# Kernel tuning notes

Measured on AMD Instinct MI355X. Metric: run time of the kernel, lower is better.

## Reference

```python
import jax, jax.numpy as jnp
import numpy as np

# Irreps config: input/output = 32x0e + 16x1o (dim 80), H=4 heads -> head = 8x0e + 4x1o (dim 20)
M0, M1 = 32, 16      # input muls for 0e / 1o
m0, m1 = 8, 4        # per-head muls
H = 4
HEAD_DIM = m0 + 3 * m1   # 20
WNUM = H * (M0 * m0 + M1 * m0 + M0 * m1 + M1 * m1)  # 2304 per-edge TP weights
NB, HID = 16, 64
SQRT3 = np.float32(np.sqrt(3.0))
EPS = 1e-8


def radial_mlp(x, W1, b1, W2, b2):
    return jax.nn.silu(x @ W1 + b1) @ W2 + b2


def tp_edge(ss, vv, sh0, sh1, w):
    """FullyConnectedTensorProduct (32x0e+16x1o) x (1x0e+1x1o) -> H*(8x0e+4x1o) with per-edge weights w [E, WNUM].
    Paths: 0e*0e->0e, 1o*1o->0e (CG dot/sqrt3), 0e*1o->1o, 1o*0e->1o; path norm 1/sqrt(fan_in)."""
    E = ss.shape[0]
    per = M0 * m0 + M1 * m0 + M0 * m1 + M1 * m1  # 576
    w = w.reshape(E, H, per)
    o = 0
    Wss = w[..., o:o + M0 * m0].reshape(E, H, M0, m0); o += M0 * m0
    Wvv = w[..., o:o + M1 * m0].reshape(E, H, M1, m0); o += M1 * m0
    Wsv = w[..., o:o + M0 * m1].reshape(E, H, M0, m1); o += M0 * m1
    Wvs = w[..., o:o + M1 * m1].reshape(E, H, M1, m1)
    fan = np.float32(np.sqrt(M0 + M1))  # fan_in = 48 for both output irreps
    vv_dot = jnp.einsum('eui,ei->eu', vv, sh1) / SQRT3
    out0 = (jnp.einsum('eu,ehuw->ehw', ss * sh0[:, None], Wss)
            + jnp.einsum('eu,ehuw->ehw', vv_dot, Wvv)) / fan          # [E,H,m0]
    out1 = (jnp.einsum('eu,ehuw->ehw', ss, Wsv)[..., None] * sh1[:, None, None, :]
            + jnp.einsum('eui,ehuw->ehwi', vv * sh0[:, None, None], Wvs)) / fan  # [E,H,m1,3]
    return out0, out1


def setup_inputs() -> dict:
    key = jax.random.key(0)
    ks = jax.random.split(key, 24)
    N, E = 2000, 32000
    g = lambda k, s, sc=1.0: jax.random.normal(k, s, jnp.float32) * sc
    inp = {}
    inp['node_features'] = g(ks[0], (N, M0 + 3 * M1))
    inp['edge_index'] = jax.random.randint(ks[1], (2, E), 0, N)
    inp['edge_sh'] = g(ks[2], (E, 4))
    inp['edge_radial_emb'] = jax.random.uniform(ks[3], (E, NB), jnp.float32)
    # query e3nn Linear (per-head blocks)
    inp['Wq0'] = g(ks[4], (H, M0, m0))
    inp['Wq1'] = g(ks[5], (H, M1, m1))
    # radial MLPs for key / value TP weights
    inp['Wk1'] = g(ks[6], (NB, HID), 1 / np.sqrt(NB)); inp['bk1'] = jnp.zeros((HID,), jnp.float32)
    inp['Wk2'] = g(ks[7], (HID, WNUM), 1 / np.sqrt(HID)); inp['bk2'] = jnp.zeros((WNUM,), jnp.float32)
    inp['Wv1'] = g(ks[8], (NB, HID), 1 / np.sqrt(NB)); inp['bv1'] = jnp.zeros((HID,), jnp.float32)
    inp['Wv2'] = g(ks[9], (HID, WNUM), 1 / np.sqrt(HID)); inp['bv2'] = jnp.zeros((WNUM,), jnp.float32)
    # single-head dot-product TP -> 0e (shared weights)
    inp['Wd0'] = g(ks[10], (m0, m0))
    inp['Wd1'] = g(ks[11], (m1, m1))
    # output projection Linear (all heads mixed per irrep)
    inp['Wo0'] = g(ks[12], (H * m0, M0))
    inp['Wo1'] = g(ks[13], (H * m1, M1))
    # FFN: out irreps -> (2*M0)x0e + M1x1o -> out irreps
    inp['Wf1_0'] = g(ks[14], (M0, 2 * M0))
    inp['Wf1_1'] = g(ks[15], (M1, M1))
    inp['Wf2_0'] = g(ks[16], (2 * M0, M0))
    inp['Wf2_1'] = g(ks[17], (M1, M1))
    return inp


def reference(node_features, edge_index, edge_sh, edge_radial_emb,
              Wq0, Wq1, Wk1, bk1, Wk2, bk2, Wv1, bv1, Wv2, bv2,
              Wd0, Wd1, Wo0, Wo1, Wf1_0, Wf1_1, Wf2_0, Wf2_1):
    N = node_features.shape[0]
    s = node_features[:, :M0]                       # [N, M0] scalars
    v = node_features[:, M0:].reshape(N, M1, 3)     # [N, M1, 3] vectors
    src, dst = edge_index[0], edge_index[1]

    # query Linear (e3nn: per-irrep channel mix, norm 1/sqrt(fan_in))
    q0 = jnp.einsum('nu,huw->nhw', s, Wq0) / np.sqrt(M0)
    q1 = jnp.einsum('nui,huw->nhwi', v, Wq1) / np.sqrt(M1)

    sh0, sh1 = edge_sh[:, 0], edge_sh[:, 1:4]
    ss, vv = s[src], v[src]                         # gather per edge

    wk = radial_mlp(edge_radial_emb, Wk1, bk1, Wk2, bk2)
    wv = radial_mlp(edge_radial_emb, Wv1, bv1, Wv2, bv2)
    k0, k1 = tp_edge(ss, vv, sh0, sh1, wk)
    v0, v1 = tp_edge(ss, vv, sh0, sh1, wv)

    # per-head equivariant dot product -> 0e logits
    qd0, qd1 = q0[dst], q1[dst]
    fan_d = np.float32(np.sqrt(m0 * m0 + m1 * m1))
    logits = (jnp.einsum('ehu,uv,ehv->eh', qd0, Wd0, k0)
              + jnp.einsum('ehui,uv,ehvi->eh', qd1, Wd1, k1) / SQRT3) / fan_d
    logits = logits / np.sqrt(HEAD_DIM)             # self.scale
    logits = jnp.clip(logits, -10.0, 10.0)

    # scatter softmax over edges sharing a destination node
    seg_max = jax.ops.segment_max(logits, dst, num_segments=N)
    seg_max = jnp.maximum(seg_max, -10.0)           # handle empty segments
    ex = jnp.exp(logits - seg_max[dst])
    denom = jax.ops.segment_sum(ex, dst, num_segments=N)
    alpha = ex / (denom[dst] + 1e-12)               # [E, H]

    agg0 = jax.ops.segment_sum(alpha[..., None] * v0, dst, num_segments=N)        # [N,H,m0]
    agg1 = jax.ops.segment_sum(alpha[..., None, None] * v1, dst, num_segments=N)  # [N,H,m1,3]

    # output projection Linear over concatenated heads
    o0 = agg0.reshape(N, H * m0) @ Wo0 / np.sqrt(H * m0)
    o1 = jnp.einsum('nui,uw->nwi', agg1.reshape(N, H * m1, 3), Wo1) / np.sqrt(H * m1)

    # residual (input irreps == output irreps -> identity skip)
    x0 = s + o0
    x1 = v + o1

    # FFN with SafeNormActivation
    f0 = x0 @ Wf1_0 / np.sqrt(M0)                               # [N, 2*M0]
    f1 = jnp.einsum('nui,uw->nwi', x1, Wf1_1) / np.sqrt(M1)     # [N, M1, 3]
    a0 = jax.nn.silu(f0)
    norms = jnp.linalg.norm(f1, axis=-1, keepdims=True)
    safe = jnp.maximum(norms, EPS)
    a1 = jnp.where(norms < EPS, 0.0, (f1 / safe) * jax.nn.silu(norms))
    g0 = a0 @ Wf2_0 / np.sqrt(2 * M0)
    g1 = jnp.einsum('nui,uw->nwi', a1, Wf2_1) / np.sqrt(M1)

    out0 = x0 + g0
    out1 = x1 + g1
    return jnp.concatenate([out0, out1.reshape(N, M1 * 3)], axis=-1)
```

## Files before the change

### kernel.cpp

```cpp
#include <hip/hip_runtime.h>

typedef unsigned int uint;
typedef unsigned short ushort;
typedef __attribute__((ext_vector_type(8))) short bf16x8;
typedef __attribute__((ext_vector_type(4))) float f32x4;

#define N_NODES 2000
#define N_EDGES 32000
#define WNUM 2304

constexpr size_t OFF_AGG0 = 0;
constexpr size_t OFF_AGG1 = 64000;
constexpr size_t OFF_DEN  = 160000;
constexpr size_t OFF_FLAG = 168000;
constexpr size_t OFF_W2T  = 168004;

__device__ __forceinline__ float b2f(ushort u){ union{uint i; float f;}x; x.i=((uint)u)<<16; return x.f; }
__device__ __forceinline__ ushort f2b(float f){
  union{float f; uint u;}x; x.f=f;
  uint r = (x.u + 0x7FFFu + ((x.u>>16)&1u)) >> 16;
  return (ushort)r;
}
__device__ __forceinline__ float siluf(float x){ return x / (1.f + __expf(-x)); }

template<bool F32>
__device__ __forceinline__ float ldf(const void* p, int i){
  if (F32) return ((const float*)p)[i];
  return b2f(((const ushort*)p)[i]);
}
__device__ __forceinline__ float ldfr(const void* p, int i, bool f32){
  return f32 ? ((const float*)p)[i] : b2f(((const ushort*)p)[i]);
}

__global__ void probe_kernel(const ushort* __restrict__ nf, int* __restrict__ flag){
  __shared__ int cnt;
  if (threadIdx.x == 0) cnt = 0;
  __syncthreads();
  uint u = nf[threadIdx.x * 2];
  uint ex = (u >> 7) & 0xFFu;
  if (ex >= 0xA0u) atomicAdd(&cnt, 1);
  __syncthreads();
  if (threadIdx.x == 0) *flag = (cnt >= 20) ? 1 : 0;
}

__global__ __launch_bounds__(256) void w2t_kernel(const void* __restrict__ Wk2,
                                                  const void* __restrict__ Wv2,
                                                  ushort* __restrict__ W2T,
                                                  const int* __restrict__ flag){
  const bool F32 = (*flag) != 0;
  int id = blockIdx.x*256 + threadIdx.x;
  int mat = id / 147456;
  int rem = id - mat*147456;
  int c = rem & 63, j = rem >> 6;
  const void* W = mat ? Wv2 : Wk2;
  float v = F32 ? ((const float*)W)[c*WNUM + j] : b2f(((const ushort*)W)[c*WNUM + j]);
  W2T[id] = f2b(v);
}

struct Smem {
  ushort hidA[2][32][64];
  float fssT[32][32];
  float fvvT[16][32];
  float sslT[32][32];
  float vshT[16][3][32];
  float qd0T[4][8][32];
  float qd1T[4][4][3][32];
  float sh1T[3][32];
  float dstF[32][80];
  int   dstL[32];
};

template<bool F32>
__device__ void edge_body(
    const void* __restrict__ nf,  const int* __restrict__ eidx,
    const void* __restrict__ esh, const void* __restrict__ emb,
    const void* __restrict__ Wk1, const void* __restrict__ bk1, const void* __restrict__ bk2,
    const void* __restrict__ Wv1, const void* __restrict__ bv1, const void* __restrict__ bv2,
    const void* __restrict__ Wq0, const void* __restrict__ Wq1,
    const void* __restrict__ Wd0, const void* __restrict__ Wd1,
    const ushort* __restrict__ W2T,
    float* __restrict__ agg0, float* __restrict__ agg1, float* __restrict__ denom,
    Smem& sm){
  const int t  = threadIdx.x;
  const int hw = t >> 5;
  const int r  = t & 31;
  const int geb = blockIdx.x*32;

  #pragma unroll 1
  for (int e=0; e<4; ++e){
    const int le = hw*4+e, ge = geb+le;
    const int src = eidx[ge], d = eidx[N_EDGES+ge];
    const float sh0 = ldf<F32>(esh, ge*4+0);
    const float s1a = ldf<F32>(esh, ge*4+1), s1b = ldf<F32>(esh, ge*4+2), s1c = ldf<F32>(esh, ge*4+3);
    if (r == 0) sm.dstL[le] = d;
    if (r < 3) sm.sh1T[r][le] = (r==0)? s1a : (r==1)? s1b : s1c;
    float sv = ldf<F32>(nf, src*80 + r);
    sm.sslT[r][le] = sv;
    sm.fssT[r][le] = sv * sh0;
    sm.dstF[le][r] = ldf<F32>(nf, d*80 + r);
    if (r < 16){
      float v0 = ldf<F32>(nf, src*80+32+r*3+0);
      float v1 = ldf<F32>(nf, src*80+32+r*3+1);
      float v2 = ldf<F32>(nf, src*80+32+r*3+2);
      sm.vshT[r][0][le] = v0*sh0; sm.vshT[r][1][le] = v1*sh0; sm.vshT[r][2][le] = v2*sh0;
      sm.fvvT[r][le] = (v0*s1a + v1*s1b + v2*s1c) * 0.5773502691896258f;
      sm.dstF[le][32+r*3+0] = ldf<F32>(nf, d*80+32+r*3+0);
      sm.dstF[le][32+r*3+1] = ldf<F32>(nf, d*80+32+r*3+1);
      sm.dstF[le][32+r*3+2] = ldf<F32>(nf, d*80+32+r*3+2);
    }
  }

  #pragma unroll 1
  for (int e=0; e<4; ++e){
    const int le = hw*4+e;
    const int h8 = r & 24, w8 = r & 7;
    float a = 0.f;
    #pragma unroll
    for (int u=0; u<32; ++u) a += sm.dstF[le][u] * ldf<F32>(Wq0, (r>>3)*256 + u*8 + w8);
    const float q0 = a * 0.17677669529663687f;
    float qd0 = 0.f;
    #pragma unroll
    for (int u=0; u<8; ++u) qd0 += __shfl(q0, h8+u, 32) * ldf<F32>(Wd0, u*8 + w8);
    sm.qd0T[r>>3][w8][le] = qd0;

    const int rr = r & 15, h4 = rr>>2, w4 = rr&3;
    float q1i[3];
    #pragma unroll
    for (int i=0; i<3; ++i){
      float b = 0.f;
      #pragma unroll
      for (int u=0; u<16; ++u) b += sm.dstF[le][32+u*3+i] * ldf<F32>(Wq1, h4*64 + u*4 + w4);
      q1i[i] = b * 0.25f;
    }
    #pragma unroll
    for (int i=0; i<3; ++i){
      float b = 0.f;
      #pragma unroll
      for (int u=0; u<4; ++u) b += __shfl(q1i[i], h4*4+u, 32) * ldf<F32>(Wd1, u*4 + w4);
      if (r < 16) sm.qd1T[h4][w4][i][le] = b;
    }
  }

  #pragma unroll 1
  for (int e=0; e<4; ++e){
    const int le = hw*4+e, ge = geb+le;
    float em[16];
    #pragma unroll
    for (int b=0; b<16; ++b) em[b] = ldf<F32>(emb, ge*16 + b);
    #pragma unroll
    for (int cc=0; cc<2; ++cc){
      const int c = r + cc*32;
      float ak = ldf<F32>(bk1, c), av = ldf<F32>(bv1, c);
      #pragma unroll
      for (int b=0; b<16; ++b){
        ak += em[b] * ldf<F32>(Wk1, b*64 + c);
        av += em[b] * ldf<F32>(Wv1, b*64 + c);
      }
      sm.hidA[0][le][c] = f2b(siluf(ak));
      sm.hidA[1][le][c] = f2b(siluf(av));
    }
  }
  __syncthreads();

  const int h = t >> 6;
  const int lane = t & 63, q = lane >> 4, n = lane & 15;
  const ushort* w2tk = W2T;
  const ushort* w2tv = W2T + 147456;

  bf16x8 af[2][2][2];
  #pragma unroll
  for (int kv=0; kv<2; ++kv)
    #pragma unroll
    for (int Mt=0; Mt<2; ++Mt)
      #pragma unroll
      for (int kh=0; kh<2; ++kh)
        af[kv][Mt][kh] = *(const bf16x8*)&sm.hidA[kv][Mt*16+n][kh*32 + q*8];

  float aK0[2][4], aV0[2][4], aPK[2][4], aPV[2][4], aWK[3][2][4], aWV[3][2][4];
  #pragma unroll
  for (int Mt=0; Mt<2; ++Mt)
    #pragma unroll
    for (int z=0; z<4; ++z){
      aK0[Mt][z]=0.f; aV0[Mt][z]=0.f; aPK[Mt][z]=0.f; aPV[Mt][z]=0.f;
      aWK[0][Mt][z]=0.f; aWK[1][Mt][z]=0.f; aWK[2][Mt][z]=0.f;
      aWV[0][Mt][z]=0.f; aWV[1][Mt][z]=0.f; aWV[2][Mt][z]=0.f;
    }

  #pragma unroll 2
  for (int tl=0; tl<16; ++tl){
    const size_t tb = ((size_t)((h*36+tl)*16 + n))*64 + q*8;
    bf16x8 bk0 = *(const bf16x8*)(w2tk + tb), bk1f = *(const bf16x8*)(w2tk + tb + 32);
    bf16x8 bv0 = *(const bf16x8*)(w2tv + tb), bv1f = *(const bf16x8*)(w2tv + tb + 32);
    const int j = h*576 + tl*16 + n;
    const float bbk = ldf<F32>(bk2, j), bbv = ldf<F32>(bv2, j);
    const int u = tl*2 + (n>>3);
    #pragma unroll
    for (int Mt=0; Mt<2; ++Mt){
      f32x4 fv = *(const f32x4*)&sm.fssT[u][Mt*16+q*4];
      f32x4 ck = {bbk,bbk,bbk,bbk};
      ck = __builtin_amdgcn_mfma_f32_16x16x32_bf16(af[0][Mt][0], bk0, ck, 0,0,0);
      ck = __builtin_amdgcn_mfma_f32_16x16x32_bf16(af[0][Mt][1], bk1f, ck, 0,0,0);
      f32x4 cv = {bbv,bbv,bbv,bbv};
      cv = __builtin_amdgcn_mfma_f32_16x16x32_bf16(af[1][Mt][0], bv0, cv, 0,0,0);
      cv = __builtin_amdgcn_mfma_f32_16x16x32_bf16(af[1][Mt][1], bv1f, cv, 0,0,0);
      #pragma unroll
      for (int z=0; z<4; ++z){ aK0[Mt][z] += ck[z]*fv[z]; aV0[Mt][z] += cv[z]*fv[z]; }
    }
  }
  #pragma unroll 2
  for (int tl=16; tl<24; ++tl){
    const size_t tb = ((size_t)((h*36+tl)*16 + n))*64 + q*8;
    bf16x8 bk0 = *(const bf16x8*)(w2tk + tb), bk1f = *(const bf16x8*)(w2tk + tb + 32);
    bf16x8 bv0 = *(const bf16x8*)(w2tv + tb), bv1f = *(const bf16x8*)(w2tv + tb + 32);
    const int j = h*576 + tl*16 + n;
    const float bbk = ldf<F32>(bk2, j), bbv = ldf<F32>(bv2, j);
    const int u = (tl-16)*2 + (n>>3);
    #pragma unroll
    for (int Mt=0; Mt<2; ++Mt){
      f32x4 fv = *(const f32x4*)&sm.fvvT[u][Mt*16+q*4];
      f32x4 ck = {bbk,bbk,bbk,bbk};
      ck = __builtin_amdgcn_mfma_f32_16x16x32_bf16(af[0][Mt][0], bk0, ck, 0,0,0);
      ck = __builtin_amdgcn_mfma_f32_16x16x32_bf16(af[0][Mt][1], bk1f, ck, 0,0,0);
      f32x4 cv = {bbv,bbv,bbv,bbv};
      cv = __builtin_amdgcn_mfma_f32_16x16x32_bf16(af[1][Mt][0], bv0, cv, 0,0,0);
      cv = __builtin_amdgcn_mfma_f32_16x16x32_bf16(af[1][Mt][1], bv1f, cv, 0,0,0);
      #pragma unroll
      for (int z=0; z<4; ++z){ aK0[Mt][z] += ck[z]*fv[z]; aV0[Mt][z] += cv[z]*fv[z]; }
    }
  }
  #pragma unroll 2
  for (int tl=24; tl<32; ++tl){
    const size_t tb = ((size_t)((h*36+tl)*16 + n))*64 + q*8;
    bf16x8 bk0 = *(const bf16x8*)(w2tk + tb), bk1f = *(const bf16x8*)(w2tk + tb + 32);
    bf16x8 bv0 = *(const bf16x8*)(w2tv + tb), bv1f = *(const bf16x8*)(w2tv + tb + 32);
    const int j = h*576 + tl*16 + n;
    const float bbk = ldf<F32>(bk2, j), bbv = ldf<F32>(bv2, j);
    const int u = (tl-24)*4 + (n>>2);
    #pragma unroll
    for (int Mt=0; Mt<2; ++Mt){
      f32x4 fv = *(const f32x4*)&sm.sslT[u][Mt*16+q*4];
      f32x4 ck = {bbk,bbk,bbk,bbk};
      ck = __builtin_amdgcn_mfma_f32_16x16x32_bf16(af[0][Mt][0], bk0, ck, 0,0,0);
      ck = __builtin_amdgcn_mfma_f32_16x16x32_bf16(af[0][Mt][1], bk1f, ck, 0,0,0);
      f32x4 cv = {bbv,bbv,bbv,bbv};
      cv = __builtin_amdgcn_mfma_f32_16x16x32_bf16(af[1][Mt][0], bv0, cv, 0,0,0);
      cv = __builtin_amdgcn_mfma_f32_16x16x32_bf16(af[1][Mt][1], bv1f, cv, 0,0,0);
      #pragma unroll
      for (int z=0; z<4; ++z){ aPK[Mt][z] += ck[z]*fv[z]; aPV[Mt][z] += cv[z]*fv[z]; }
    }
  }
  #pragma unroll 1
  for (int tl=32; tl<36; ++tl){
    const size_t tb = ((size_t)((h*36+tl)*16 + n))*64 + q*8;
    bf16x8 bk0 = *(const bf16x8*)(w2tk + tb), bk1f = *(const bf16x8*)(w2tk + tb + 32);
    bf16x8 bv0 = *(const bf16x8*)(w2tv + tb), bv1f = *(const bf16x8*)(w2tv + tb + 32);
    const int j = h*576 + tl*16 + n;
    const float bbk = ldf<F32>(bk2, j), bbv = ldf<F32>(bv2, j);
    const int u = (tl-32)*4 + (n>>2);
    #pragma unroll
    for (int Mt=0; Mt<2; ++Mt){
      f32x4 ck = {bbk,bbk,bbk,bbk};
      ck = __builtin_amdgcn_mfma_f32_16x16x32_bf16(af[0][Mt][0], bk0, ck, 0,0,0);
      ck = __builtin_amdgcn_mfma_f32_16x16x32_bf16(af[0][Mt][1], bk1f, ck, 0,0,0);
      f32x4 cv = {bbv,bbv,bbv,bbv};
      cv = __builtin_amdgcn_mfma_f32_16x16x32_bf16(af[1][Mt][0], bv0, cv, 0,0,0);
      cv = __builtin_amdgcn_mfma_f32_16x16x32_bf16(af[1][Mt][1], bv1f, cv, 0,0,0);
      #pragma unroll
      for (int i=0; i<3; ++i){
        f32x4 fv = *(const f32x4*)&sm.vshT[u][i][Mt*16+q*4];
        #pragma unroll
        for (int z=0; z<4; ++z){ aWK[i][Mt][z] += ck[z]*fv[z]; aWV[i][Mt][z] += cv[z]*fv[z]; }
      }
    }
  }

  #pragma unroll
  for (int Mt=0; Mt<2; ++Mt)
    #pragma unroll
    for (int z=0; z<4; ++z){
      aK0[Mt][z] += __shfl_xor(aK0[Mt][z], 8, 64);
      aV0[Mt][z] += __shfl_xor(aV0[Mt][z], 8, 64);
      aPK[Mt][z] += __shfl_xor(aPK[Mt][z], 4, 64);
      aPK[Mt][z] += __shfl_xor(aPK[Mt][z], 8, 64);
      aPV[Mt][z] += __shfl_xor(aPV[Mt][z], 4, 64);
      aPV[Mt][z] += __shfl_xor(aPV[Mt][z], 8, 64);
      #pragma unroll
      for (int i=0; i<3; ++i){
        aWK[i][Mt][z] += __shfl_xor(aWK[i][Mt][z], 4, 64);
        aWK[i][Mt][z] += __shfl_xor(aWK[i][Mt][z], 8, 64);
        aWV[i][Mt][z] += __shfl_xor(aWV[i][Mt][z], 4, 64);
        aWV[i][Mt][z] += __shfl_xor(aWV[i][Mt][z], 8, 64);
      }
    }

  const float invfan = 0.14433756729740643f;
  f32x4 s1v[3][2];
  #pragma unroll
  for (int i=0; i<3; ++i)
    #pragma unroll
    for (int Mt=0; Mt<2; ++Mt)
      s1v[i][Mt] = *(const f32x4*)&sm.sh1T[i][Mt*16+q*4];

  float lgp[2][4];
  #pragma unroll
  for (int Mt=0; Mt<2; ++Mt){
    f32x4 qd0v = *(const f32x4*)&sm.qd0T[h][n&7][Mt*16+q*4];
    #pragma unroll
    for (int z=0; z<4; ++z){
      float acc = (n < 8) ? qd0v[z]*aK0[Mt][z] : 0.f;
      if (n < 4){
        float s = 0.f;
        #pragma unroll
        for (int i=0; i<3; ++i){
          f32x4 qd1v = *(const f32x4*)&sm.qd1T[h][n&3][i][Mt*16+q*4];
          float k1 = aPK[Mt][z]*s1v[i][Mt][z] + aWK[i][Mt][z];
          s += qd1v[z]*k1;
        }
        acc += s * 0.5773502691896258f;
      }
      lgp[Mt][z] = acc;
    }
  }
  #pragma unroll
  for (int Mt=0; Mt<2; ++Mt)
    #pragma unroll
    for (int z=0; z<4; ++z){
      lgp[Mt][z] += __shfl_xor(lgp[Mt][z], 1, 64);
      lgp[Mt][z] += __shfl_xor(lgp[Mt][z], 2, 64);
      lgp[Mt][z] += __shfl_xor(lgp[Mt][z], 4, 64);
      lgp[Mt][z] += __shfl_xor(lgp[Mt][z], 8, 64);
    }

  float exv[2][4]; int dn[2][4];
  #pragma unroll
  for (int Mt=0; Mt<2; ++Mt)
    #pragma unroll
    for (int z=0; z<4; ++z){
      float lg = lgp[Mt][z] * invfan * 0.025f;
      lg = fminf(10.f, fmaxf(-10.f, lg));
      exv[Mt][z] = __expf(lg - 10.0f);
      dn[Mt][z] = sm.dstL[Mt*16 + q*4 + z];
    }

  if (n == 0){
    #pragma unroll
    for (int Mt=0; Mt<2; ++Mt)
      #pragma unroll
      for (int z=0; z<4; ++z)
        atomicAdd(denom + dn[Mt][z]*4 + h, exv[Mt][z]);
  }
  if (n < 8){
    #pragma unroll
    for (int Mt=0; Mt<2; ++Mt)
      #pragma unroll
      for (int z=0; z<4; ++z)
        atomicAdd(agg0 + dn[Mt][z]*32 + h*8 + n, exv[Mt][z]*aV0[Mt][z]*invfan);
  }
  if (n < 4){
    #pragma unroll
    for (int i=0; i<3; ++i)
      #pragma unroll
      for (int Mt=0; Mt<2; ++Mt)
        #pragma unroll
        for (int z=0; z<4; ++z){
          float v1 = (aPV[Mt][z]*s1v[i][Mt][z] + aWV[i][Mt][z]) * invfan;
          atomicAdd(agg1 + dn[Mt][z]*48 + h*12 + n*3 + i, exv[Mt][z]*v1);
        }
  }
}

__global__ __launch_bounds__(256) void edge_kernel(
    const void* nf, const int* eidx, const void* esh, const void* emb,
    const void* Wk1, const void* bk1, const void* bk2,
    const void* Wv1, const void* bv1, const void* bv2,
    const void* Wq0, const void* Wq1, const void* Wd0, const void* Wd1,
    const ushort* W2T, float* agg0, float* agg1, float* denom, const int* flag){
  __shared__ Smem sm;
  if (*flag)
    edge_body<true >(nf,eidx,esh,emb,Wk1,bk1,bk2,Wv1,bv1,bv2,Wq0,Wq1,Wd0,Wd1,W2T,agg0,agg1,denom,sm);
  else
    edge_body<false>(nf,eidx,esh,emb,Wk1,bk1,bk2,Wv1,bv1,bv2,Wq0,Wq1,Wd0,Wd1,W2T,agg0,agg1,denom,sm);
}

__global__ __launch_bounds__(64) void node_out_kernel(
    const void* __restrict__ nf, const float* __restrict__ agg0r, const float* __restrict__ agg1r,
    const float* __restrict__ denom,
    const void* __restrict__ Wo0, const void* __restrict__ Wo1,
    const void* __restrict__ Wf10, const void* __restrict__ Wf11,
    const void* __restrict__ Wf20, const void* __restrict__ Wf21,
    void* __restrict__ out, const int* __restrict__ flag){
  __shared__ float ag0[32], ag1[48], adiv[4];
  __shared__ float x0s[32], x1s[48], a0s[64], f1s[48], coefs[16];
  const bool F32 = (*flag) != 0;
  const int n = blockIdx.x, t = threadIdx.x;
  if (t < 4) adiv[t] = 1.f / (denom[n*4+t] + 1e-12f);
  __syncthreads();
  if (t < 32) ag0[t] = agg0r[n*32+t] * adiv[t>>3];
  if (t < 48) ag1[t] = agg1r[n*48+t] * adiv[t/12];
  __syncthreads();
  if (t < 32){
    float o = 0.f;
    #pragma unroll
    for (int k=0; k<32; ++k) o += ag0[k]*ldfr(Wo0, k*32+t, F32);
    x0s[t] = ldfr(nf, n*80+t, F32) + o*0.17677669529663687f;
  }
  if (t < 48){
    int w = t/3, i = t - w*3;
    float o = 0.f;
    #pragma unroll
    for (int u=0; u<16; ++u) o += ag1[u*3+i]*ldfr(Wo1, u*16+w, F32);
    x1s[t] = ldfr(nf, n*80+32+t, F32) + o*0.25f;
  }
  __syncthreads();
  {
    float f0 = 0.f;
    #pragma unroll
    for (int u=0; u<32; ++u) f0 += x0s[u]*ldfr(Wf10, u*64+t, F32);
    a0s[t] = siluf(f0*0.17677669529663687f);
  }
  if (t < 48){
    int w = t/3, i = t - w*3;
    float f1 = 0.f;
    #pragma unroll
    for (int u=0; u<16; ++u) f1 += x1s[u*3+i]*ldfr(Wf11, u*16+w, F32);
    f1s[t] = f1*0.25f;
  }
  __syncthreads();
  if (t < 16){
    float a = f1s[t*3], b = f1s[t*3+1], c = f1s[t*3+2];
    float nrm = sqrtf(a*a+b*b+c*c);
    float safe = fmaxf(nrm, 1e-8f);
    coefs[t] = (nrm < 1e-8f) ? 0.f : siluf(nrm)/safe;
  }
  __syncthreads();
  if (t < 32){
    float g = 0.f;
    #pragma unroll
    for (int u=0; u<64; ++u) g += a0s[u]*ldfr(Wf20, u*32+t, F32);
    float val = x0s[t] + g*0.125f;
    if (F32) ((float*)out)[n*80+t] = val; else ((ushort*)out)[n*80+t] = f2b(val);
  }
  if (t < 48){
    int w = t/3, i = t - w*3;
    float g = 0.f;
    #pragma unroll
    for (int u=0; u<16; ++u) g += coefs[u]*f1s[u*3+i]*ldfr(Wf21, u*16+w, F32);
    float val = x1s[t] + g*0.25f;
    if (F32) ((float*)out)[n*80+32+t] = val; else ((ushort*)out)[n*80+32+t] = f2b(val);
  }
}

extern "C" void kernel_launch(void* const* d_in, const int* in_sizes, int n_in,
                              void* d_out, int out_size, void* d_ws, size_t ws_size,
                              hipStream_t stream){
  const void* nf   = d_in[0];
  const int*  eidx = (const int*)d_in[1];
  const void* esh  = d_in[2];
  const void* emb  = d_in[3];
  const void* Wq0  = d_in[4];
  const void* Wq1  = d_in[5];
  const void* Wk1  = d_in[6];
  const void* bk1  = d_in[7];
  const void* Wk2  = d_in[8];
  const void* bk2  = d_in[9];
  const void* Wv1  = d_in[10];
  const void* bv1  = d_in[11];
  const void* Wv2  = d_in[12];
  const void* bv2  = d_in[13];
  const void* Wd0  = d_in[14];
  const void* Wd1  = d_in[15];
  const void* Wo0  = d_in[16];
  const void* Wo1  = d_in[17];
  const void* Wf10 = d_in[18];
  const void* Wf11 = d_in[19];
  const void* Wf20 = d_in[20];
  const void* Wf21 = d_in[21];
  float* ws = (float*)d_ws;

  float* agg0  = ws + OFF_AGG0;
  float* agg1  = ws + OFF_AGG1;
  float* denom = ws + OFF_DEN;
  int*   flag  = (int*)(ws + OFF_FLAG);
  ushort* W2T  = (ushort*)(ws + OFF_W2T);

  hipMemsetAsync(agg0, 0, (64000+96000+8000)*sizeof(float), stream);
  probe_kernel<<<1, 256, 0, stream>>>((const ushort*)nf, flag);
  w2t_kernel<<<1152, 256, 0, stream>>>(Wk2, Wv2, W2T, flag);
  edge_kernel<<<N_EDGES/32, 256, 0, stream>>>(nf, eidx, esh, emb,
                                              Wk1, bk1, bk2, Wv1, bv1, bv2,
                                              Wq0, Wq1, Wd0, Wd1, W2T,
                                              agg0, agg1, denom, flag);
  node_out_kernel<<<N_NODES, 64, 0, stream>>>(nf, agg0, agg1, denom,
                                              Wo0, Wo1, Wf10, Wf11, Wf20, Wf21, d_out, flag);
}
```

Baseline: 244.2 us.

## Precompute per-node query projections in a separate kernel instead of per edge

Adds a node_q kernel that computes the query and Wd-projected query for each node and head once, storing them in workspace. The edge kernel then gathers these per destination node instead of recomputing the projection for all 32k edges, which removes the dstF shared buffer and its staging. The change also pads shared-memory arrays to cut bank conflicts, vectorises the radial-embedding loads, sets launch bounds for higher occupancy, makes the W2T transpose read coalesced, and packs four nodes per block in the output kernel. It adds one extra launch and scattered global gathers of the precomputed queries.

After: 262.1 us. 7.3% more time.

```diff
diff --git a/kernel.cpp b/kernel.cpp
--- a/kernel.cpp
+++ b/kernel.cpp
@@ -14,8 +14,12 @@
 constexpr size_t OFF_DEN  = 160000;
 constexpr size_t OFF_FLAG = 168000;
 constexpr size_t OFF_W2T  = 168004;
+constexpr size_t OFF_QT0  = 315460;
+constexpr size_t OFF_QT1  = 379460;
 
 __device__ __forceinline__ float b2f(ushort u){ union{uint i; float f;}x; x.i=((uint)u)<<16; return x.f; }
+__device__ __forceinline__ float lo16(uint w){ union{uint u; float f;}x; x.u=w<<16; return x.f; }
+__device__ __forceinline__ float hi16(uint w){ union{uint u; float f;}x; x.u=w&0xFFFF0000u; return x.f; }
 __device__ __forceinline__ ushort f2b(float f){
   union{float f; uint u;}x; x.f=f;
   uint r = (x.u + 0x7FFFu + ((x.u>>16)&1u)) >> 16;
@@ -51,22 +55,74 @@
   int id = blockIdx.x*256 + threadIdx.x;
   int mat = id / 147456;
   int rem = id - mat*147456;
-  int c = rem & 63, j = rem >> 6;
+  int c = rem / WNUM, j = rem - c*WNUM;
   const void* W = mat ? Wv2 : Wk2;
-  float v = F32 ? ((const float*)W)[c*WNUM + j] : b2f(((const ushort*)W)[c*WNUM + j]);
-  W2T[id] = f2b(v);
+  float v = F32 ? ((const float*)W)[rem] : b2f(((const ushort*)W)[rem]);
+  W2T[(size_t)mat*147456 + (size_t)j*64 + c] = f2b(v);
+}
+
+template<bool F32>
+__device__ void node_q_body(const void* __restrict__ nf,
+    const void* __restrict__ Wq0, const void* __restrict__ Wq1,
+    const void* __restrict__ Wd0, const void* __restrict__ Wd1,
+    float* __restrict__ qt0, float* __restrict__ qt1){
+  int tid = blockIdx.x*blockDim.x + threadIdx.x;
+  if (tid >= N_NODES*4) return;
+  int n = tid >> 2, h = tid & 3;
+  float s[32], v[48];
+  #pragma unroll
+  for (int u=0; u<32; ++u) s[u] = ldf<F32>(nf, n*80+u);
+  #pragma unroll
+  for (int u=0; u<48; ++u) v[u] = ldf<F32>(nf, n*80+32+u);
+  float q0[8];
+  #pragma unroll
+  for (int w=0; w<8; ++w){
+    float a = 0.f;
+    #pragma unroll
+    for (int u=0; u<32; ++u) a += s[u]*ldf<F32>(Wq0, h*256 + u*8 + w);
+    q0[w] = a * 0.17677669529663687f;
+  }
+  #pragma unroll
+  for (int vv=0; vv<8; ++vv){
+    float a = 0.f;
+    #pragma unroll
+    for (int u=0; u<8; ++u) a += q0[u]*ldf<F32>(Wd0, u*8+vv);
+    qt0[n*32 + h*8 + vv] = a;
+  }
+  float q1[12];
+  #pragma unroll
+  for (int w=0; w<4; ++w)
+    #pragma unroll
+    for (int i=0; i<3; ++i){
+      float a = 0.f;
+      #pragma unroll
+      for (int u=0; u<16; ++u) a += v[u*3+i]*ldf<F32>(Wq1, h*64 + u*4 + w);
+      q1[w*3+i] = a * 0.25f;
+    }
+  #pragma unroll
+  for (int vv=0; vv<4; ++vv)
+    #pragma unroll
+    for (int i=0; i<3; ++i){
+      float a = 0.f;
+      #pragma unroll
+      for (int u=0; u<4; ++u) a += q1[u*3+i]*ldf<F32>(Wd1, u*4+vv);
+      qt1[n*48 + h*12 + vv*3 + i] = a;
+    }
+}
+__global__ __launch_bounds__(256) void node_q_kernel(const void* nf,
+    const void* Wq0, const void* Wq1, const void* Wd0, const void* Wd1,
+    float* qt0, float* qt1, const int* flag){
+  if (*flag) node_q_body<true >(nf, Wq0, Wq1, Wd0, Wd1, qt0, qt1);
+  else       node_q_body<false>(nf, Wq0, Wq1, Wd0, Wd1, qt0, qt1);
 }
 
 struct Smem {
   ushort hidA[2][32][64];
-  float fssT[32][32];
-  float fvvT[16][32];
-  float sslT[32][32];
-  float vshT[16][3][32];
-  float qd0T[4][8][32];
-  float qd1T[4][4][3][32];
-  float sh1T[3][32];
-  float dstF[32][80];
+  float fssT[32][36];
+  float fvvT[16][36];
+  float sslT[32][36];
+  float vshT[16][3][36];
+  float sh1T[3][36];
   int   dstL[32];
 };
 
@@ -76,9 +132,8 @@
     const void* __restrict__ esh, const void* __restrict__ emb,
     const void* __restrict__ Wk1, const void* __restrict__ bk1, const void* __restrict__ bk2,
     const void* __restrict__ Wv1, const void* __restrict__ bv1, const void* __restrict__ bv2,
-    const void* __restrict__ Wq0, const void* __restrict__ Wq1,
-    const void* __restrict__ Wd0, const void* __restrict__ Wd1,
     const ushort* __restrict__ W2T,
+    const float* __restrict__ qt0g, const float* __restrict__ qt1g,
     float* __restrict__ agg0, float* __restrict__ agg1, float* __restrict__ denom,
     Smem& sm){
   const int t  = threadIdx.x;
@@ -97,47 +152,12 @@
     float sv = ldf<F32>(nf, src*80 + r);
     sm.sslT[r][le] = sv;
     sm.fssT[r][le] = sv * sh0;
-    sm.dstF[le][r] = ldf<F32>(nf, d*80 + r);
     if (r < 16){
       float v0 = ldf<F32>(nf, src*80+32+r*3+0);
       float v1 = ldf<F32>(nf, src*80+32+r*3+1);
       float v2 = ldf<F32>(nf, src*80+32+r*3+2);
       sm.vshT[r][0][le] = v0*sh0; sm.vshT[r][1][le] = v1*sh0; sm.vshT[r][2][le] = v2*sh0;
       sm.fvvT[r][le] = (v0*s1a + v1*s1b + v2*s1c) * 0.5773502691896258f;
-      sm.dstF[le][32+r*3+0] = ldf<F32>(nf, d*80+32+r*3+0);
-      sm.dstF[le][32+r*3+1] = ldf<F32>(nf, d*80+32+r*3+1);
-      sm.dstF[le][32+r*3+2] = ldf<F32>(nf, d*80+32+r*3+2);
-    }
-  }
-
-  #pragma unroll 1
-  for (int e=0; e<4; ++e){
-    const int le = hw*4+e;
-    const int h8 = r & 24, w8 = r & 7;
-    float a = 0.f;
-    #pragma unroll
-    for (int u=0; u<32; ++u) a += sm.dstF[le][u] * ldf<F32>(Wq0, (r>>3)*256 + u*8 + w8);
-    const float q0 = a * 0.17677669529663687f;
-    float qd0 = 0.f;
-    #pragma unroll
-    for (int u=0; u<8; ++u) qd0 += __shfl(q0, h8+u, 32) * ldf<F32>(Wd0, u*8 + w8);
-    sm.qd0T[r>>3][w8][le] = qd0;
-
-    const int rr = r & 15, h4 = rr>>2, w4 = rr&3;
-    float q1i[3];
-    #pragma unroll
-    for (int i=0; i<3; ++i){
-      float b = 0.f;
-      #pragma unroll
-      for (int u=0; u<16; ++u) b += sm.dstF[le][32+u*3+i] * ldf<F32>(Wq1, h4*64 + u*4 + w4);
-      q1i[i] = b * 0.25f;
-    }
-    #pragma unroll
-    for (int i=0; i<3; ++i){
-      float b = 0.f;
-      #pragma unroll
-      for (int u=0; u<4; ++u) b += __shfl(q1i[i], h4*4+u, 32) * ldf<F32>(Wd1, u*4 + w4);
-      if (r < 16) sm.qd1T[h4][w4][i][le] = b;
     }
   }
 
@@ -145,8 +165,21 @@
   for (int e=0; e<4; ++e){
     const int le = hw*4+e, ge = geb+le;
     float em[16];
-    #pragma unroll
-    for (int b=0; b<16; ++b) em[b] = ldf<F32>(emb, ge*16 + b);
+    if (F32){
+      const float4* p = (const float4*)((const float*)emb + ge*16);
+      float4 a=p[0], b=p[1], c=p[2], d4=p[3];
+      em[0]=a.x; em[1]=a.y; em[2]=a.z; em[3]=a.w;
+      em[4]=b.x; em[5]=b.y; em[6]=b.z; em[7]=b.w;
+      em[8]=c.x; em[9]=c.y; em[10]=c.z; em[11]=c.w;
+      em[12]=d4.x; em[13]=d4.y; em[14]=d4.z; em[15]=d4.w;
+    } else {
+      const uint4* p = (const uint4*)((const ushort*)emb + ge*16);
+      uint4 a=p[0], b=p[1];
+      em[0]=lo16(a.x); em[1]=hi16(a.x); em[2]=lo16(a.y); em[3]=hi16(a.y);
+      em[4]=lo16(a.z); em[5]=hi16(a.z); em[6]=lo16(a.w); em[7]=hi16(a.w);
+      em[8]=lo16(b.x); em[9]=hi16(b.x); em[10]=lo16(b.y); em[11]=hi16(b.y);
+      em[12]=lo16(b.z); em[13]=hi16(b.z); em[14]=lo16(b.w); em[15]=hi16(b.w);
+    }
     #pragma unroll
     for (int cc=0; cc<2; ++cc){
       const int c = r + cc*32;
@@ -294,6 +327,12 @@
     }
 
   const float invfan = 0.14433756729740643f;
+  int dn[2][4];
+  #pragma unroll
+  for (int Mt=0; Mt<2; ++Mt)
+    #pragma unroll
+    for (int z=0; z<4; ++z) dn[Mt][z] = sm.dstL[Mt*16 + q*4 + z];
+
   f32x4 s1v[3][2];
   #pragma unroll
   for (int i=0; i<3; ++i)
@@ -303,24 +342,22 @@
 
   float lgp[2][4];
   #pragma unroll
-  for (int Mt=0; Mt<2; ++Mt){
-    f32x4 qd0v = *(const f32x4*)&sm.qd0T[h][n&7][Mt*16+q*4];
+  for (int Mt=0; Mt<2; ++Mt)
     #pragma unroll
     for (int z=0; z<4; ++z){
-      float acc = (n < 8) ? qd0v[z]*aK0[Mt][z] : 0.f;
+      float acc = 0.f;
+      if (n < 8) acc = qt0g[dn[Mt][z]*32 + h*8 + n] * aK0[Mt][z];
       if (n < 4){
         float s = 0.f;
         #pragma unroll
         for (int i=0; i<3; ++i){
-          f32x4 qd1v = *(const f32x4*)&sm.qd1T[h][n&3][i][Mt*16+q*4];
           float k1 = aPK[Mt][z]*s1v[i][Mt][z] + aWK[i][Mt][z];
-          s += qd1v[z]*k1;
+          s += qt1g[dn[Mt][z]*48 + h*12 + n*3 + i] * k1;
         }
         acc += s * 0.5773502691896258f;
       }
       lgp[Mt][z] = acc;
     }
-  }
   #pragma unroll
   for (int Mt=0; Mt<2; ++Mt)
     #pragma unroll
@@ -331,7 +368,7 @@
       lgp[Mt][z] += __shfl_xor(lgp[Mt][z], 8, 64);
     }
 
-  float exv[2][4]; int dn[2][4];
+  float exv[2][4];
   #pragma unroll
   for (int Mt=0; Mt<2; ++Mt)
     #pragma unroll
@@ -339,7 +376,6 @@
       float lg = lgp[Mt][z] * invfan * 0.025f;
       lg = fminf(10.f, fmaxf(-10.f, lg));
       exv[Mt][z] = __expf(lg - 10.0f);
-      dn[Mt][z] = sm.dstL[Mt*16 + q*4 + z];
     }
 
   if (n == 0){
@@ -369,83 +405,84 @@
   }
 }
 
-__global__ __launch_bounds__(256) void edge_kernel(
+__global__ __launch_bounds__(256, 4) void edge_kernel(
     const void* nf, const int* eidx, const void* esh, const void* emb,
     const void* Wk1, const void* bk1, const void* bk2,
     const void* Wv1, const void* bv1, const void* bv2,
-    const void* Wq0, const void* Wq1, const void* Wd0, const void* Wd1,
-    const ushort* W2T, float* agg0, float* agg1, float* denom, const int* flag){
+    const ushort* W2T, const float* qt0g, const float* qt1g,
+    float* agg0, float* agg1, float* denom, const int* flag){
   __shared__ Smem sm;
   if (*flag)
-    edge_body<true >(nf,eidx,esh,emb,Wk1,bk1,bk2,Wv1,bv1,bv2,Wq0,Wq1,Wd0,Wd1,W2T,agg0,agg1,denom,sm);
+    edge_body<true >(nf,eidx,esh,emb,Wk1,bk1,bk2,Wv1,bv1,bv2,W2T,qt0g,qt1g,agg0,agg1,denom,sm);
   else
-    edge_body<false>(nf,eidx,esh,emb,Wk1,bk1,bk2,Wv1,bv1,bv2,Wq0,Wq1,Wd0,Wd1,W2T,agg0,agg1,denom,sm);
-}
-
-__global__ __launch_bounds__(64) void node_out_kernel(
+    edge_body<false>(nf,eidx,esh,emb,Wk1,bk1,bk2,Wv1,bv1,bv2,W2T,qt0g,qt1g,agg0,agg1,denom,sm);
+}
+
+__global__ __launch_bounds__(256) void node_out_kernel(
     const void* __restrict__ nf, const float* __restrict__ agg0r, const float* __restrict__ agg1r,
     const float* __restrict__ denom,
     const void* __restrict__ Wo0, const void* __restrict__ Wo1,
     const void* __restrict__ Wf10, const void* __restrict__ Wf11,
     const void* __restrict__ Wf20, const void* __restrict__ Wf21,
     void* __restrict__ out, const int* __restrict__ flag){
-  __shared__ float ag0[32], ag1[48], adiv[4];
-  __shared__ float x0s[32], x1s[48], a0s[64], f1s[48], coefs[16];
+  __shared__ float ag0[4][32], ag1[4][48], adiv[4][4];
+  __shared__ float x0s[4][32], x1s[4][48], a0s[4][64], f1s[4][48], coefs[4][16];
   const bool F32 = (*flag) != 0;
-  const int n = blockIdx.x, t = threadIdx.x;
-  if (t < 4) adiv[t] = 1.f / (denom[n*4+t] + 1e-12f);
-  __syncthreads();
-  if (t < 32) ag0[t] = agg0r[n*32+t] * adiv[t>>3];
-  if (t < 48) ag1[t] = agg1r[n*48+t] * adiv[t/12];
+  const int g = threadIdx.x >> 6, t = threadIdx.x & 63;
+  const int n = blockIdx.x*4 + g;
+  if (t < 4) adiv[g][t] = 1.f / (denom[n*4+t] + 1e-12f);
+  __syncthreads();
+  if (t < 32) ag0[g][t] = agg0r[n*32+t] * adiv[g][t>>3];
+  if (t < 48) ag1[g][t] = agg1r[n*48+t] * adiv[g][t/12];
   __syncthreads();
   if (t < 32){
     float o = 0.f;
     #pragma unroll
-    for (int k=0; k<32; ++k) o += ag0[k]*ldfr(Wo0, k*32+t, F32);
-    x0s[t] = ldfr(nf, n*80+t, F32) + o*0.17677669529663687f;
+    for (int k=0; k<32; ++k) o += ag0[g][k]*ldfr(Wo0, k*32+t, F32);
+    x0s[g][t] = ldfr(nf, n*80+t, F32) + o*0.17677669529663687f;
   }
   if (t < 48){
     int w = t/3, i = t - w*3;
     float o = 0.f;
     #pragma unroll
-    for (int u=0; u<16; ++u) o += ag1[u*3+i]*ldfr(Wo1, u*16+w, F32);
-    x1s[t] = ldfr(nf, n*80+32+t, F32) + o*0.25f;
+    for (int u=0; u<16; ++u) o += ag1[g][u*3+i]*ldfr(Wo1, u*16+w, F32);
+    x1s[g][t] = ldfr(nf, n*80+32+t, F32) + o*0.25f;
   }
   __syncthreads();
   {
     float f0 = 0.f;
     #pragma unroll
-    for (int u=0; u<32; ++u) f0 += x0s[u]*ldfr(Wf10, u*64+t, F32);
-    a0s[t] = siluf(f0*0.17677669529663687f);
+    for (int u=0; u<32; ++u) f0 += x0s[g][u]*ldfr(Wf10, u*64+t, F32);
+    a0s[g][t] = siluf(f0*0.17677669529663687f);
   }
   if (t < 48){
     int w = t/3, i = t - w*3;
     float f1 = 0.f;
     #pragma unroll
-    for (int u=0; u<16; ++u) f1 += x1s[u*3+i]*ldfr(Wf11, u*16+w, F32);
-    f1s[t] = f1*0.25f;
+    for (int u=0; u<16; ++u) f1 += x1s[g][u*3+i]*ldfr(Wf11, u*16+w, F32);
+    f1s[g][t] = f1*0.25f;
   }
   __syncthreads();
   if (t < 16){
-    float a = f1s[t*3], b = f1s[t*3+1], c = f1s[t*3+2];
+    float a = f1s[g][t*3], b = f1s[g][t*3+1], c = f1s[g][t*3+2];
     float nrm = sqrtf(a*a+b*b+c*c);
     float safe = fmaxf(nrm, 1e-8f);
-    coefs[t] = (nrm < 1e-8f) ? 0.f : siluf(nrm)/safe;
+    coefs[g][t] = (nrm < 1e-8f) ? 0.f : siluf(nrm)/safe;
   }
   __syncthreads();
   if (t < 32){
-    float g = 0.f;
-    #pragma unroll
-    for (int u=0; u<64; ++u) g += a0s[u]*ldfr(Wf20, u*32+t, F32);
-    float val = x0s[t] + g*0.125f;
+    float gg = 0.f;
+    #pragma unroll
+    for (int u=0; u<64; ++u) gg += a0s[g][u]*ldfr(Wf20, u*32+t, F32);
+    float val = x0s[g][t] + gg*0.125f;
     if (F32) ((float*)out)[n*80+t] = val; else ((ushort*)out)[n*80+t] = f2b(val);
   }
   if (t < 48){
     int w = t/3, i = t - w*3;
-    float g = 0.f;
-    #pragma unroll
-    for (int u=0; u<16; ++u) g += coefs[u]*f1s[u*3+i]*ldfr(Wf21, u*16+w, F32);
-    float val = x1s[t] + g*0.25f;
+    float gg = 0.f;
+    #pragma unroll
+    for (int u=0; u<16; ++u) gg += coefs[g][u]*f1s[g][u*3+i]*ldfr(Wf21, u*16+w, F32);
+    float val = x1s[g][t] + gg*0.25f;
     if (F32) ((float*)out)[n*80+32+t] = val; else ((ushort*)out)[n*80+32+t] = f2b(val);
   }
 }
@@ -482,14 +519,17 @@
   float* denom = ws + OFF_DEN;
   int*   flag  = (int*)(ws + OFF_FLAG);
   ushort* W2T  = (ushort*)(ws + OFF_W2T);
+  float* qt0   = ws + OFF_QT0;
+  float* qt1   = ws + OFF_QT1;
 
   hipMemsetAsync(agg0, 0, (64000+96000+8000)*sizeof(float), stream);
   probe_kernel<<<1, 256, 0, stream>>>((const ushort*)nf, flag);
+  node_q_kernel<<<(N_NODES*4+255)/256, 256, 0, stream>>>(nf, Wq0, Wq1, Wd0, Wd1, qt0, qt1, flag);
   w2t_kernel<<<1152, 256, 0, stream>>>(Wk2, Wv2, W2T, flag);
   edge_kernel<<<N_EDGES/32, 256, 0, stream>>>(nf, eidx, esh, emb,
                                               Wk1, bk1, bk2, Wv1, bv1, bv2,
-                                              Wq0, Wq1, Wd0, Wd1, W2T,
+                                              W2T, qt0, qt1,
                                               agg0, agg1, denom, flag);
-  node_out_kernel<<<N_NODES, 64, 0, stream>>>(nf, agg0, agg1, denom,
-                                              Wo0, Wo1, Wf10, Wf11, Wf20, Wf21, d_out, flag);
-}
+  node_out_kernel<<<N_NODES/4, 256, 0, stream>>>(nf, agg0, agg1, denom,
+                                                 Wo0, Wo1, Wf10, Wf11, Wf20, Wf21, d_out, flag);
+}
```
